# Kernel optimization log

Hardware: AMD Instinct MI355X
Metric: run time of the kernel (lower is better)

The kernel has to match this reference:

```python
import jax, jax.numpy as jnp
import numpy as np

DN = ('NCH', 'OIH', 'NCH')  # conv dimension numbers: [batch, channel, length]

def setup_inputs() -> dict:
    key = jax.random.key(0)
    ks = jax.random.split(key, 8)
    B, S, L, D, F, V = 16, 64, 128, 512, 256, 30000
    return {
        'text': jax.random.randint(ks[0], (B, S, L), 0, V),
        'embed': jax.random.normal(ks[1], (V, D), dtype=jnp.float32),
        'w3': jax.random.normal(ks[2], (F, D, 3), dtype=jnp.float32) * 0.05,
        'b3': jax.random.normal(ks[3], (F,), dtype=jnp.float32) * 0.05,
        'w4': jax.random.normal(ks[4], (F, D, 4), dtype=jnp.float32) * 0.05,
        'b4': jax.random.normal(ks[5], (F,), dtype=jnp.float32) * 0.05,
        'w5': jax.random.normal(ks[6], (F, D, 5), dtype=jnp.float32) * 0.05,
        'b5': jax.random.normal(ks[7], (F,), dtype=jnp.float32) * 0.05,
    }

def reference(text, embed, w3, b3, w4, b4, w5, b5):
    B, S, L = text.shape
    # Embed tokens, flatten episodes x utterances into one batch, channels-first.
    x = embed[text]                                   # [B, S, L, D]
    x = x.reshape(B * S, L, -1).transpose(0, 2, 1)    # [BS, D, L]
    outs = []
    for w, b in ((w3, b3), (w4, b4), (w5, b5)):
        y = jax.lax.conv_general_dilated(x, w, (1,), 'VALID', dimension_numbers=DN)
        # max-over-time pooling (valid conv -> length L-K+1)
        outs.append(jnp.max(y + b[None, :, None], axis=2))  # [BS, F]
    out = jax.nn.relu(jnp.concatenate(outs, axis=1))  # [BS, 3F]
    return out.reshape(B, S, -1)
```

## Files before the change

### kernel.cpp

```cpp
#include <hip/hip_runtime.h>
#include <hip/hip_bf16.h>


typedef __bf16 bf16x8 __attribute__((ext_vector_type(8)));
typedef float f32x4 __attribute__((ext_vector_type(4)));
typedef float f32x16 __attribute__((ext_vector_type(16)));

#define ROWS 132
#define ROWB 512
#define BUF_BYTES (ROWS * ROWB)
#define RED_OFF (2 * BUF_BYTES)
#define LDS_TOTAL (RED_OFF + 4096)
#define WQ_ELEMS 1572864

__global__ void pack_w_kernel(const float* __restrict__ w3,
                              const float* __restrict__ w4,
                              const float* __restrict__ w5,
                              __bf16* __restrict__ wq) {
    const int t    = blockIdx.x * 256 + threadIdx.x;
    const int g    = t >> 6;
    const int lane = t & 63;
    int rel, Kw; const float* w;
    if (g < 768)       { rel = g;        Kw = 3; w = w3; }
    else if (g < 1792) { rel = g - 768;  Kw = 4; w = w4; }
    else               { rel = g - 1792; Kw = 5; w = w5; }
    const int k16 = rel >> 3;
    const int n32 = rel & 7;
    const int f   = n32 * 32 + (lane & 31);
    const int tap = k16 >> 5;
    const int d0  = (k16 & 31) * 16 + (lane >> 5) * 8;
    const float* src = w + ((size_t)f * 512 + d0) * Kw + tap;
    bf16x8 o;
#pragma unroll
    for (int j = 0; j < 8; ++j) o[j] = (__bf16)src[j * Kw];
    *(bf16x8*)(wq + (size_t)t * 8) = o;
}

__global__ __launch_bounds__(1024, 4) void conv_gemm_kernel(
        const int* __restrict__ text,
        const float* __restrict__ embed,
        const __bf16* __restrict__ wq,
        const float* __restrict__ b3,
        const float* __restrict__ b4,
        const float* __restrict__ b5,
        float* __restrict__ out) {
    extern __shared__ char lds[];
    float* const red = (float*)(lds + RED_OFF);

    const int tid  = threadIdx.x;
    const int lane = tid & 63;
    const int wave = tid >> 6;
    const int wm   = wave & 3;
    const int wn   = wave >> 2;
    const int l31  = lane & 31;
    const int lh   = lane >> 5;
    const int sr   = tid >> 5;
    const int sc   = tid & 31;

    const int bsbase = blockIdx.x * 4;

    float4 G[4];
    auto issuePair = [&](int nbs, int h, int p0) {
#pragma unroll
        for (int p = 0; p < 2; ++p) {
            const int r = (p0 + p) * 32 + sr;
            const int tok = text[nbs * 128 + r];
            const float* src = embed + (size_t)tok * 512 + h * 256 + sc * 8;
            G[p * 2]     = *(const float4*)(src);
            G[p * 2 + 1] = *(const float4*)(src + 4);
        }
    };
    auto writePair = [&](char* bufp, int p0) {
#pragma unroll
        for (int p = 0; p < 2; ++p) {
            const int r = (p0 + p) * 32 + sr;
            const float4 v0 = G[p * 2], v1 = G[p * 2 + 1];
            bf16x8 o;
            o[0] = (__bf16)v0.x; o[1] = (__bf16)v0.y;
            o[2] = (__bf16)v0.z; o[3] = (__bf16)v0.w;
            o[4] = (__bf16)v1.x; o[5] = (__bf16)v1.y;
            o[6] = (__bf16)v1.z; o[7] = (__bf16)v1.w;
            *(bf16x8*)(bufp + r * ROWB + (((sc ^ (r & 7))) << 4)) = o;
        }
    };

    f32x16 acc[2];
    bf16x8 Br[4][2];
    const __bf16* const bpL = wq + (size_t)wn * 1024 + (size_t)lane * 8;

    issuePair(bsbase, 0, 0); writePair(lds, 0);
    issuePair(bsbase, 0, 2); writePair(lds, 2);
    issuePair(bsbase, 1, 0); writePair(lds + BUF_BYTES, 0);
    issuePair(bsbase, 1, 2); writePair(lds + BUF_BYTES, 2);
    if (tid < 128) {
        const int r = 128 + sr;
        const int off = r * ROWB + ((sc ^ (r & 7)) << 4);
        bf16x8 z = {};
        *(bf16x8*)(lds + off) = z;
        *(bf16x8*)(lds + BUF_BYTES + off) = z;
    }
#pragma unroll
    for (int k = 0; k < 4; ++k) {
        Br[k][0] = *(const bf16x8*)(bpL + k * 4096);
        Br[k][1] = *(const bf16x8*)(bpL + k * 4096 + 512);
    }
    __syncthreads();

#pragma unroll 1
    for (int i = 0; i < 4; ++i) {
        const int bs  = bsbase + i;
        const int nbs = bs + 1;
        const bool stg = (i < 3);
#pragma unroll 1
        for (int c = 0; c < 3; ++c) {
            const int KW = 3 + c;
            const size_t cb  = (c == 0) ? 0 : (c == 1) ? 393216 : 917504;
            const size_t cbn = (c == 2) ? 0 : (c == 0) ? 393216 : 917504;
            const __bf16* bpc = bpL + cb;
            const __bf16* bpn = bpL + cbn;
            const bool lastc = stg && (c == 2);
#pragma unroll
            for (int r = 0; r < 16; ++r) { acc[0][r] = 0.f; acc[1][r] = 0.f; }

            if (lastc) issuePair(nbs, 0, 0);

            const int arow = wm * 32 + l31;
            bf16x8 a_cur = *(const bf16x8*)(
                lds + arow * 512 + ((lh ^ (arow & 7)) << 4));

#pragma unroll 1
            for (int h = 0; h < 2; ++h) {
                const int hb = h * 16;
                const int bo = h ? BUF_BYTES : 0;
#pragma unroll 1
                for (int tap = 0; tap < KW; ++tap) {
                    const int row = arow + tap;
                    const int v   = row & 7;
                    const int rb  = bo + row * 512;
                    int P[4];
#pragma unroll
                    for (int k = 0; k < 4; ++k)
                        P[k] = rb + (((k * 2 + lh) ^ v) << 4);
                    int R0;
                    if (tap < KW - 1) {
                        const int r2 = row + 1;
                        R0 = bo + r2 * 512 + ((lh ^ (r2 & 7)) << 4);
                    } else if (h == 0) {
                        R0 = BUF_BYTES + arow * 512 + ((lh ^ (arow & 7)) << 4);
                    } else R0 = P[0];
                    const int t1 = tap * 32 + hb + 4;
                    int t2; bool pn = false;
                    if (tap < KW - 1)  t2 = tap * 32 + hb + 20;
                    else if (h == 0)   t2 = 4;
                    else             { t2 = -12; pn = true; }
#pragma unroll
                    for (int s = 0; s < 16; ++s) {
                        const bf16x8 a_n = *(const bf16x8*)(lds +
                            ((s < 15) ? P[(s + 1) & 3] + (((s + 1) >> 2) << 7)
                                      : R0));
                        __builtin_amdgcn_s_setprio(1);
                        acc[0] = __builtin_amdgcn_mfma_f32_32x32x16_bf16(
                            a_cur, Br[s & 3][0], acc[0], 0, 0, 0);
                        acc[1] = __builtin_amdgcn_mfma_f32_32x32x16_bf16(
                            a_cur, Br[s & 3][1], acc[1], 0, 0, 0);
                        __builtin_amdgcn_s_setprio(0);
                        const int tk = (s < 12) ? (t1 + s) : (t2 + s);
                        const __bf16* p =
                            (((s >= 12) && pn) ? bpn : bpc) + (size_t)tk * 4096;
                        Br[s & 3][0] = *(const bf16x8*)(p);
                        Br[s & 3][1] = *(const bf16x8*)(p + 512);
                        a_cur = a_n;
                    }
                }
                if (h == 0 && lastc) {
                    __syncthreads();
                    writePair(lds, 0);
                    issuePair(nbs, 0, 2);
                    writePair(lds, 2);
                    issuePair(nbs, 1, 0);
                }
            }

            const int Tv = 126 - c;
            float cmax[2];
#pragma unroll
            for (int nt = 0; nt < 2; ++nt) {
                float mx = -3.0e38f;
#pragma unroll
                for (int r = 0; r < 16; ++r) {
                    const int t = wm * 32 + (r & 3) + 8 * (r >> 2) + 4 * lh;
                    if (t < Tv) mx = fmaxf(mx, acc[nt][r]);
                }
                mx = fmaxf(mx, __shfl_xor(mx, 32, 64));
                cmax[nt] = mx;
            }
            __syncthreads();
            if (lastc) {
                writePair(lds + BUF_BYTES, 0);
                issuePair(nbs, 1, 2);
                writePair(lds + BUF_BYTES, 2);
            }
            if (lane < 32) {
                red[wm * 256 + wn * 64 + l31]      = cmax[0];
                red[wm * 256 + wn * 64 + 32 + l31] = cmax[1];
            }
            __syncthreads();
            if (tid < 256) {
                const float* bias = (c == 0) ? b3 : (c == 1) ? b4 : b5;
                const float vv = fmaxf(fmaxf(red[tid], red[256 + tid]),
                                       fmaxf(red[512 + tid], red[768 + tid]))
                                 + bias[tid];
                out[(size_t)bs * 768 + c * 256 + tid] = fmaxf(vv, 0.f);
            }
        }
    }
}

extern "C" void kernel_launch(void* const* d_in, const int* in_sizes, int n_in,
                              void* d_out, int out_size, void* d_ws, size_t ws_size,
                              hipStream_t stream) {
    const int*   text  = (const int*)d_in[0];
    const float* embed = (const float*)d_in[1];
    const float* w3    = (const float*)d_in[2];
    const float* b3    = (const float*)d_in[3];
    const float* w4    = (const float*)d_in[4];
    const float* b4    = (const float*)d_in[5];
    const float* w5    = (const float*)d_in[6];
    const float* b5    = (const float*)d_in[7];
    float* out = (float*)d_out;

    __bf16* wq = (__bf16*)d_ws;

    (void)hipFuncSetAttribute((const void*)conv_gemm_kernel,
                              hipFuncAttributeMaxDynamicSharedMemorySize,
                              LDS_TOTAL);

    pack_w_kernel<<<768, 256, 0, stream>>>(w3, w4, w5, wq);
    conv_gemm_kernel<<<256, 1024, LDS_TOTAL, stream>>>(text, embed, wq,
                                                       b3, b4, b5, out);
}
```

Measured before the change: 533.9 us.

## Retile waves to 64x32 output tiles and restructure tap/half loop ordering

Changes the wave decomposition from 4x4 (32 rows x 64 filters per wave) to 2x8 (64 rows x 32 filters per wave), so each wave loads two A fragments from LDS and one B fragment from global per step instead of one A and two B. The loop is reordered to tap-outer, half-inner, with a new XOR swizzle for A addressing. Staging of the next batch item is moved entirely to after the final reduction, and embedding loads and output stores use nontemporal hints. This halves per-wave global weight traffic, at the cost of doubled LDS A reads, less overlap of next-item staging with compute, and a shrunk reduction buffer.

After: 496.5 us. 7.0% less time.

```diff
diff --git a/kernel.cpp b/kernel.cpp
--- a/kernel.cpp
+++ b/kernel.cpp
@@ -3,15 +3,14 @@
 
 
 typedef __bf16 bf16x8 __attribute__((ext_vector_type(8)));
-typedef float f32x4 __attribute__((ext_vector_type(4)));
 typedef float f32x16 __attribute__((ext_vector_type(16)));
+typedef float f32x4v __attribute__((ext_vector_type(4)));
 
 #define ROWS 132
 #define ROWB 512
 #define BUF_BYTES (ROWS * ROWB)
 #define RED_OFF (2 * BUF_BYTES)
-#define LDS_TOTAL (RED_OFF + 4096)
-#define WQ_ELEMS 1572864
+#define LDS_TOTAL (RED_OFF + 2048)
 
 __global__ void pack_w_kernel(const float* __restrict__ w3,
                               const float* __restrict__ w4,
@@ -50,8 +49,8 @@
     const int tid  = threadIdx.x;
     const int lane = tid & 63;
     const int wave = tid >> 6;
-    const int wm   = wave & 3;
-    const int wn   = wave >> 2;
+    const int wm   = wave & 1;
+    const int wn   = wave >> 1;
     const int l31  = lane & 31;
     const int lh   = lane >> 5;
     const int sr   = tid >> 5;
@@ -59,34 +58,41 @@
 
     const int bsbase = blockIdx.x * 4;
 
-    float4 G[4];
+    const int arow = wm * 64 + l31;
+    const int av   = arow & 7;
+    const int A00  = arow * 512 + ((av >> 1) << 5) + ((lh ^ (av & 1)) << 4);
+
+    const __bf16* const bpL = wq + (size_t)wn * 512 + (size_t)lane * 8;
+
+    f32x4v G[4];
     auto issuePair = [&](int nbs, int h, int p0) {
 #pragma unroll
         for (int p = 0; p < 2; ++p) {
             const int r = (p0 + p) * 32 + sr;
             const int tok = text[nbs * 128 + r];
-            const float* src = embed + (size_t)tok * 512 + h * 256 + sc * 8;
-            G[p * 2]     = *(const float4*)(src);
-            G[p * 2 + 1] = *(const float4*)(src + 4);
+            const f32x4v* src = (const f32x4v*)
+                (embed + (size_t)tok * 512 + h * 256 + sc * 8);
+            G[p * 2]     = __builtin_nontemporal_load(src);
+            G[p * 2 + 1] = __builtin_nontemporal_load(src + 1);
         }
     };
     auto writePair = [&](char* bufp, int p0) {
 #pragma unroll
         for (int p = 0; p < 2; ++p) {
             const int r = (p0 + p) * 32 + sr;
-            const float4 v0 = G[p * 2], v1 = G[p * 2 + 1];
+            const f32x4v v0 = G[p * 2], v1 = G[p * 2 + 1];
             bf16x8 o;
             o[0] = (__bf16)v0.x; o[1] = (__bf16)v0.y;
             o[2] = (__bf16)v0.z; o[3] = (__bf16)v0.w;
             o[4] = (__bf16)v1.x; o[5] = (__bf16)v1.y;
             o[6] = (__bf16)v1.z; o[7] = (__bf16)v1.w;
-            *(bf16x8*)(bufp + r * ROWB + (((sc ^ (r & 7))) << 4)) = o;
+            *(bf16x8*)(bufp + r * ROWB + ((sc ^ (r & 7)) << 4)) = o;
         }
     };
 
     f32x16 acc[2];
-    bf16x8 Br[4][2];
-    const __bf16* const bpL = wq + (size_t)wn * 1024 + (size_t)lane * 8;
+    bf16x8 Br[4];
+    bf16x8 a0, a1;
 
     issuePair(bsbase, 0, 0); writePair(lds, 0);
     issuePair(bsbase, 0, 2); writePair(lds, 2);
@@ -100,10 +106,8 @@
         *(bf16x8*)(lds + BUF_BYTES + off) = z;
     }
 #pragma unroll
-    for (int k = 0; k < 4; ++k) {
-        Br[k][0] = *(const bf16x8*)(bpL + k * 4096);
-        Br[k][1] = *(const bf16x8*)(bpL + k * 4096 + 512);
-    }
+    for (int k = 0; k < 4; ++k)
+        Br[k] = *(const bf16x8*)(bpL + (size_t)k * 4096);
     __syncthreads();
 
 #pragma unroll 1
@@ -115,102 +119,88 @@
         for (int c = 0; c < 3; ++c) {
             const int KW = 3 + c;
             const size_t cb  = (c == 0) ? 0 : (c == 1) ? 393216 : 917504;
-            const size_t cbn = (c == 2) ? 0 : (c == 0) ? 393216 : 917504;
+            const size_t cbn = (c == 0) ? 393216 : (c == 1) ? 917504 : 0;
             const __bf16* bpc = bpL + cb;
             const __bf16* bpn = bpL + cbn;
             const bool lastc = stg && (c == 2);
+
 #pragma unroll
             for (int r = 0; r < 16; ++r) { acc[0][r] = 0.f; acc[1][r] = 0.f; }
 
             if (lastc) issuePair(nbs, 0, 0);
 
-            const int arow = wm * 32 + l31;
-            bf16x8 a_cur = *(const bf16x8*)(
-                lds + arow * 512 + ((lh ^ (arow & 7)) << 4));
+            a0 = *(const bf16x8*)(lds + A00);
+            a1 = *(const bf16x8*)(lds + A00 + 16384);
 
 #pragma unroll 1
-            for (int h = 0; h < 2; ++h) {
-                const int hb = h * 16;
-                const int bo = h ? BUF_BYTES : 0;
-#pragma unroll 1
-                for (int tap = 0; tap < KW; ++tap) {
-                    const int row = arow + tap;
-                    const int v   = row & 7;
-                    const int rb  = bo + row * 512;
-                    int P[4];
-#pragma unroll
-                    for (int k = 0; k < 4; ++k)
-                        P[k] = rb + (((k * 2 + lh) ^ v) << 4);
-                    int R0;
-                    if (tap < KW - 1) {
-                        const int r2 = row + 1;
-                        R0 = bo + r2 * 512 + ((lh ^ (r2 & 7)) << 4);
-                    } else if (h == 0) {
-                        R0 = BUF_BYTES + arow * 512 + ((lh ^ (arow & 7)) << 4);
-                    } else R0 = P[0];
-                    const int t1 = tap * 32 + hb + 4;
-                    int t2; bool pn = false;
-                    if (tap < KW - 1)  t2 = tap * 32 + hb + 20;
-                    else if (h == 0)   t2 = 4;
-                    else             { t2 = -12; pn = true; }
-#pragma unroll
-                    for (int s = 0; s < 16; ++s) {
-                        const bf16x8 a_n = *(const bf16x8*)(lds +
-                            ((s < 15) ? P[(s + 1) & 3] + (((s + 1) >> 2) << 7)
-                                      : R0));
+            for (int tap = 0; tap < KW; ++tap) {
+                const int row = arow + tap;
+                const int v = row & 7, u = v >> 1;
+                const int Base = row * 512 + ((lh ^ (v & 1)) << 4);
+                int P[4];
+#pragma unroll
+                for (int r = 0; r < 4; ++r) P[r] = Base + ((r ^ u) << 5);
+                const int r2 = row + 1, v2 = r2 & 7;
+                const int NT0 = r2 * 512 + ((v2 >> 1) << 5)
+                                         + ((lh ^ (v2 & 1)) << 4);
+#pragma unroll
+                for (int dh = 0; dh < 2; ++dh) {
+                    const int bo = dh ? BUF_BYTES : 0;
+                    const int s0 = tap * 32 + dh * 16;
+                    const __bf16* q0 = bpc + (size_t)(s0 + 4) * 4096;
+                    const __bf16* q1 = (dh == 1 && tap == KW - 1)
+                                           ? bpn : (q0 + 12 * 4096);
+#pragma unroll
+                    for (int d = 0; d < 16; ++d) {
+                        int na;
+                        if (d < 15)
+                            na = bo + P[(d + 1) & 3] + (((d + 1) >> 2) << 7);
+                        else if (dh == 0)
+                            na = BUF_BYTES + P[0];
+                        else
+                            na = NT0;
+                        const bf16x8 n0 = *(const bf16x8*)(lds + na);
+                        const bf16x8 n1 = *(const bf16x8*)(lds + na + 16384);
                         __builtin_amdgcn_s_setprio(1);
                         acc[0] = __builtin_amdgcn_mfma_f32_32x32x16_bf16(
-                            a_cur, Br[s & 3][0], acc[0], 0, 0, 0);
+                            a0, Br[d & 3], acc[0], 0, 0, 0);
                         acc[1] = __builtin_amdgcn_mfma_f32_32x32x16_bf16(
-                            a_cur, Br[s & 3][1], acc[1], 0, 0, 0);
+                            a1, Br[d & 3], acc[1], 0, 0, 0);
                         __builtin_amdgcn_s_setprio(0);
-                        const int tk = (s < 12) ? (t1 + s) : (t2 + s);
-                        const __bf16* p =
-                            (((s >= 12) && pn) ? bpn : bpc) + (size_t)tk * 4096;
-                        Br[s & 3][0] = *(const bf16x8*)(p);
-                        Br[s & 3][1] = *(const bf16x8*)(p + 512);
-                        a_cur = a_n;
+                        Br[d & 3] = (d < 12)
+                            ? *(const bf16x8*)(q0 + (size_t)d * 4096)
+                            : *(const bf16x8*)(q1 + (size_t)(d - 12) * 4096);
+                        a0 = n0; a1 = n1;
                     }
                 }
-                if (h == 0 && lastc) {
-                    __syncthreads();
-                    writePair(lds, 0);
-                    issuePair(nbs, 0, 2);
-                    writePair(lds, 2);
-                    issuePair(nbs, 1, 0);
+            }
+
+            const int Tv = 126 - c;
+            float cmax = -3.0e38f;
+#pragma unroll
+            for (int mt = 0; mt < 2; ++mt)
+#pragma unroll
+                for (int r = 0; r < 16; ++r) {
+                    const int t = wm * 64 + mt * 32
+                                + (r & 3) + 8 * (r >> 2) + 4 * lh;
+                    if (t < Tv) cmax = fmaxf(cmax, acc[mt][r]);
                 }
-            }
-
-            const int Tv = 126 - c;
-            float cmax[2];
-#pragma unroll
-            for (int nt = 0; nt < 2; ++nt) {
-                float mx = -3.0e38f;
-#pragma unroll
-                for (int r = 0; r < 16; ++r) {
-                    const int t = wm * 32 + (r & 3) + 8 * (r >> 2) + 4 * lh;
-                    if (t < Tv) mx = fmaxf(mx, acc[nt][r]);
-                }
-                mx = fmaxf(mx, __shfl_xor(mx, 32, 64));
-                cmax[nt] = mx;
-            }
+            cmax = fmaxf(cmax, __shfl_xor(cmax, 32, 64));
+
             __syncthreads();
+            if (lane < 32) red[wm * 256 + wn * 32 + l31] = cmax;
             if (lastc) {
-                writePair(lds + BUF_BYTES, 0);
-                issuePair(nbs, 1, 2);
-                writePair(lds + BUF_BYTES, 2);
-            }
-            if (lane < 32) {
-                red[wm * 256 + wn * 64 + l31]      = cmax[0];
-                red[wm * 256 + wn * 64 + 32 + l31] = cmax[1];
+                writePair(lds, 0);
+                issuePair(nbs, 0, 2); writePair(lds, 2);
+                issuePair(nbs, 1, 0); writePair(lds + BUF_BYTES, 0);
+                issuePair(nbs, 1, 2); writePair(lds + BUF_BYTES, 2);
             }
             __syncthreads();
             if (tid < 256) {
                 const float* bias = (c == 0) ? b3 : (c == 1) ? b4 : b5;
-                const float vv = fmaxf(fmaxf(red[tid], red[256 + tid]),
-                                       fmaxf(red[512 + tid], red[768 + tid]))
-                                 + bias[tid];
-                out[(size_t)bs * 768 + c * 256 + tid] = fmaxf(vv, 0.f);
+                const float vv = fmaxf(red[tid], red[256 + tid]) + bias[tid];
+                __builtin_nontemporal_store(fmaxf(vv, 0.f),
+                    &out[(size_t)bs * 768 + c * 256 + tid]);
             }
         }
     }
```
